# Optimization experiments

Hardware: AMD Instinct MI355X
Metric: run time of the kernel (lower is better)

Reference implementation:

```python
import jax, jax.numpy as jnp
import numpy as np

EPS = 1e-5

def layer_norm(x, g, b):
    m = jnp.mean(x, axis=-1, keepdims=True)
    v = jnp.var(x, axis=-1, keepdims=True)
    return (x - m) / jnp.sqrt(v + EPS) * g + b

def mab(Q, K, adj, Wq, Wk, Wv, Wo, g1, b1, g2, b2, H):
    # Q: [B, nq, dq], K: [B, nk, dk], adj: [nk, nk] graph-conv aggregation
    B, nq, _ = Q.shape
    dv = Wq.shape[1]
    dh = dv // H
    Qp = Q @ Wq                                   # [B, nq, dv]
    Kg = jnp.einsum('ij,bjd->bid', adj, K)        # GCN neighborhood aggregation
    Kp = Kg @ Wk                                  # [B, nk, dv]
    Vp = Kg @ Wv                                  # [B, nk, dv]
    Qh = Qp.reshape(B, nq, H, dh)
    Kh = Kp.reshape(B, -1, H, dh)
    Vh = Vp.reshape(B, -1, H, dh)
    scale = 1.0 / np.sqrt(dv).astype(np.float32)
    att = jax.nn.softmax(jnp.einsum('bqhd,bkhd->bhqk', Qh, Kh) * scale, axis=-1)
    Oh = Qh + jnp.einsum('bhqk,bkhd->bqhd', att, Vh)   # residual inside heads
    O = Oh.reshape(B, nq, dv)
    O = layer_norm(O, g1, b1)
    O = O + jax.nn.relu(O @ Wo)
    O = layer_norm(O, g2, b2)
    return O

def setup_inputs() -> dict:
    key = jax.random.key(0)
    ks = jax.random.split(key, 16)
    B, P, D = 16384, 25, 256
    w = lambda k, shp: jax.random.normal(k, shp, dtype=jnp.float32) * 0.05
    adj2 = jax.random.uniform(ks[15], (3, 3), dtype=jnp.float32)
    adj2 = adj2 / jnp.sum(adj2, axis=-1, keepdims=True)  # row-normalized GCN adj
    return {
        'X': jax.random.normal(ks[0], (B, 1, D), dtype=jnp.float32),
        'S1': w(ks[1], (3, 1)),
        'S2': w(ks[2], (P, 3)),
        'adj1': jnp.ones((1, 1), dtype=jnp.float32),
        'adj2': adj2,
        'Wq1': w(ks[3], (D, D)), 'Wk1': w(ks[4], (D, D)),
        'Wv1': w(ks[5], (D, D)), 'Wo1': w(ks[6], (D, D)),
        'g11': jnp.ones((D,), jnp.float32), 'b11': jnp.zeros((D,), jnp.float32),
        'g12': jnp.ones((D,), jnp.float32), 'b12': jnp.zeros((D,), jnp.float32),
        'Wq2': w(ks[7], (D, D)), 'Wk2': w(ks[8], (D, D)),
        'Wv2': w(ks[9], (D, D)), 'Wo2': w(ks[10], (D, D)),
        'g21': jnp.ones((D,), jnp.float32), 'b21': jnp.zeros((D,), jnp.float32),
        'g22': jnp.ones((D,), jnp.float32), 'b22': jnp.zeros((D,), jnp.float32),
        'H': 4,
    }

def reference(X, S1, S2, adj1, adj2,
              Wq1, Wk1, Wv1, Wo1, g11, b11, g12, b12,
              Wq2, Wk2, Wv2, Wo2, g21, b21, g22, b22, H):
    Q1 = jnp.einsum('ij,bjd->bid', S1, X)            # [B, 3, D]
    scale_liner = mab(Q1, X, adj1, Wq1, Wk1, Wv1, Wo1, g11, b11, g12, b12, H)
    Q2 = jnp.einsum('pj,bjd->bpd', S2, scale_liner)  # [B, 25, D]
    scale_graph = mab(Q2, scale_liner, adj2, Wq2, Wk2, Wv2, Wo2, g21, b21, g22, b22, H)
    return scale_graph
```

## Files before the change

### kernel.cpp

```cpp
#include <hip/hip_runtime.h>


typedef __attribute__((ext_vector_type(8))) short bf16x8;
typedef __attribute__((ext_vector_type(4))) float f32x4;

constexpr int D   = 256;
constexpr int AST = 264;
constexpr int SST = 264;

__device__ __forceinline__ short f2bf(float f) {
  unsigned u = __builtin_bit_cast(unsigned, f);
  u = (u + 0x7FFFu + ((u >> 16) & 1u)) >> 16;
  return (short)u;
}
__device__ __forceinline__ float bf2f(short s) {
  unsigned u = ((unsigned)(unsigned short)s) << 16;
  return __builtin_bit_cast(float, u);
}

__global__ void pack_weights(const float* __restrict__ Wq1, const float* __restrict__ Wv1,
                             const float* __restrict__ Wo1, const float* __restrict__ Wq2,
                             const float* __restrict__ Wk2, const float* __restrict__ Wv2,
                             const float* __restrict__ Wo2, short* __restrict__ ws) {
  int g = blockIdx.x * 256 + threadIdx.x;
  int mat = g >> 13, r = g & 8191;
  const float* W = (mat == 0) ? Wq1 : (mat == 1) ? Wv1 : (mat == 2) ? Wo1 :
                   (mat == 3) ? Wq2 : (mat == 4) ? Wk2 : (mat == 5) ? Wv2 : Wo2;
  int nt = r >> 9, s = (r >> 6) & 7, lane = r & 63;
  int qd = lane >> 4, mc = lane & 15;
  bf16x8 v;
#pragma unroll
  for (int j = 0; j < 8; ++j) {
    int k = s * 32 + qd * 8 + j;
    v[j] = f2bf(W[k * 256 + nt * 16 + mc]);
  }
  *reinterpret_cast<bf16x8*>(ws + (size_t)g * 8) = v;
}

template <int MT, int NTW, bool PMODE, bool SYNCMID>
__device__ __forceinline__ void wave_gemm(const short* __restrict__ ub,
                                          const bf16x8* __restrict__ Bp, int nt0,
                                          int lane, short* __restrict__ dst,
                                          int dstStride, int lim) {
  const int m = lane & 15, q = lane >> 4;
  f32x4 acc[MT][NTW];
#pragma unroll
  for (int mt = 0; mt < MT; ++mt)
#pragma unroll
    for (int n = 0; n < NTW; ++n) acc[mt][n] = (f32x4){0.f, 0.f, 0.f, 0.f};

#pragma unroll
  for (int s = 0; s < 8; ++s) {
    bf16x8 a[MT];
#pragma unroll
    for (int mt = 0; mt < MT; ++mt)
      a[mt] = *reinterpret_cast<const bf16x8*>(ub + (mt * 16 + m) * AST + s * 32 + q * 8);
#pragma unroll
    for (int n = 0; n < NTW; ++n) {
      bf16x8 b = Bp[(nt0 + n) * 512 + s * 64 + lane];
#pragma unroll
      for (int mt = 0; mt < MT; ++mt)
        acc[mt][n] = __builtin_amdgcn_mfma_f32_16x16x32_bf16(a[mt], b, acc[mt][n], 0, 0, 0);
    }
  }
  if (SYNCMID) __syncthreads();
#pragma unroll
  for (int mt = 0; mt < MT; ++mt)
#pragma unroll
    for (int n = 0; n < NTW; ++n)
#pragma unroll
      for (int r = 0; r < 4; ++r) {
        int rr = mt * 16 + q * 4 + r;
        bool ok = PMODE ? ((rr & 31) < 25) : (rr < lim);
        if (ok) dst[rr * dstStride + (nt0 + n) * 16 + m] = f2bf(acc[mt][n][r]);
      }
}

__device__ __forceinline__ void gemm_qkv(const short* __restrict__ ub,
                                         const bf16x8* __restrict__ Bp, int nt0,
                                         int lane, short* __restrict__ sb) {
  const int m = lane & 15, q = lane >> 4;
  f32x4 acc[12];
#pragma unroll
  for (int n = 0; n < 12; ++n) acc[n] = (f32x4){0.f, 0.f, 0.f, 0.f};
#pragma unroll
  for (int s = 0; s < 8; ++s) {
    bf16x8 a = *reinterpret_cast<const bf16x8*>(ub + m * AST + s * 32 + q * 8);
#pragma unroll
    for (int n = 0; n < 12; ++n) {
      bf16x8 b = Bp[(nt0 + n) * 512 + s * 64 + lane];
      acc[n] = __builtin_amdgcn_mfma_f32_16x16x32_bf16(a, b, acc[n], 0, 0, 0);
    }
  }
#pragma unroll
  for (int n = 0; n < 12; ++n) {
    int nt = nt0 + n;
    int mat = nt >> 4;
    int lo = (mat == 0) ? 0 : 6;
    int col = (nt & 15) * 16 + m;
#pragma unroll
    for (int r = 0; r < 4; ++r) {
      int rr = q * 4 + r;
      if (rr >= lo && rr < lo + 6)
        sb[(mat * 6 + rr - lo) * SST + col] = f2bf(acc[n][r]);
    }
  }
}

__device__ __forceinline__ void ln6(float (&v)[2][3], const float* __restrict__ g,
                                    const float* __restrict__ b, int tid, float* red) {
  const int lane = tid & 63, wv = tid >> 6;
#pragma unroll
  for (int i = 0; i < 6; ++i) {
    float x = v[i / 3][i % 3];
    float s = x, qq = x * x;
#pragma unroll
    for (int mm = 32; mm; mm >>= 1) {
      s += __shfl_xor(s, mm, 64);
      qq += __shfl_xor(qq, mm, 64);
    }
    if (lane == 0) {
      red[(i * 4 + wv) * 2 + 0] = s;
      red[(i * 4 + wv) * 2 + 1] = qq;
    }
  }
  __syncthreads();
  const float gg = g[tid], bb = b[tid];
#pragma unroll
  for (int i = 0; i < 6; ++i) {
    float s = red[(i * 4 + 0) * 2] + red[(i * 4 + 1) * 2] +
              red[(i * 4 + 2) * 2] + red[(i * 4 + 3) * 2];
    float qq = red[(i * 4 + 0) * 2 + 1] + red[(i * 4 + 1) * 2 + 1] +
               red[(i * 4 + 2) * 2 + 1] + red[(i * 4 + 3) * 2 + 1];
    float mean = s * (1.0f / 256.0f);
    float var  = qq * (1.0f / 256.0f) - mean * mean;
    float inv  = rsqrtf(var + 1e-5f);
    float x = v[i / 3][i % 3];
    v[i / 3][i % 3] = (x - mean) * inv * gg + bb;
  }
  __syncthreads();
}

__device__ __forceinline__ void coop_stats(const short* __restrict__ ub, int tid,
                                           float* red, float (*st)[2]) {
  const int rr = tid >> 2, part = tid & 3;
  float s = 0.f, ss = 0.f;
  if ((rr & 31) < 25) {
#pragma unroll
    for (int c = 0; c < 8; ++c) {
      bf16x8 v8 = *reinterpret_cast<const bf16x8*>(ub + rr * AST + part * 64 + c * 8);
#pragma unroll
      for (int j = 0; j < 8; ++j) {
        float f = bf2f(v8[j]);
        s += f;
        ss = fmaf(f, f, ss);
      }
    }
  }
  red[(rr * 4 + part) * 2 + 0] = s;
  red[(rr * 4 + part) * 2 + 1] = ss;
  __syncthreads();
  if (tid < 64) {
    float S = 0.f, SS = 0.f;
#pragma unroll
    for (int i = 0; i < 4; ++i) {
      S  += red[(tid * 4 + i) * 2 + 0];
      SS += red[(tid * 4 + i) * 2 + 1];
    }
    float mean = S * (1.0f / 256.0f);
    float var  = SS * (1.0f / 256.0f) - mean * mean;
    st[tid][0] = mean;
    st[tid][1] = rsqrtf(var + 1e-5f);
  }
}

__global__ __launch_bounds__(256, 3)
void gt_mfma(const float* __restrict__ X, const float* __restrict__ S1,
             const float* __restrict__ S2, const float* __restrict__ adj1,
             const float* __restrict__ adj2,
             const float* __restrict__ g11, const float* __restrict__ b11,
             const float* __restrict__ g12, const float* __restrict__ b12,
             const float* __restrict__ g21, const float* __restrict__ b21,
             const float* __restrict__ g22, const float* __restrict__ b22,
             const short* __restrict__ wsp, float* __restrict__ out) {
  __shared__ __align__(16) short ubuf[64 * AST];
  __shared__ __align__(16) short sbuf[18 * SST];
  __shared__ __align__(16) float wbuf[4][64][4];
  __shared__ float slkbuf[4][6][3];
  __shared__ float stbuf[64][2];
  __shared__ float redbuf[512];

  const int tid = threadIdx.x, lane = tid & 63, wv = tid >> 6;
  const int b0 = blockIdx.x * 2;

  const bf16x8* pQV1 = (const bf16x8*)(wsp + 0 * 65536);
  const bf16x8* pWo1 = (const bf16x8*)(wsp + 2 * 65536);
  const bf16x8* pQKV = (const bf16x8*)(wsp + 3 * 65536);
  const bf16x8* pWo2 = (const bf16x8*)(wsp + 6 * 65536);

  short* qv = sbuf + 6 * SST;

  float x0 = X[(size_t)(b0 + 0) * D + tid];
  float x1 = X[(size_t)(b0 + 1) * D + tid];
  ubuf[0 * AST + tid] = f2bf(x0);
  ubuf[1 * AST + tid] = f2bf(x1);
  __syncthreads();

  wave_gemm<1, 8, false, false>(ubuf, pQV1, wv * 8, lane, qv, 528, 2);
  __syncthreads();

  const float a1 = adj1[0];
  float o1[2][3];
#pragma unroll
  for (int b = 0; b < 2; ++b) {
    float xq = bf2f(qv[b * 528 + tid]);
    float xv = bf2f(qv[b * 528 + 256 + tid]) * a1;
#pragma unroll
    for (int qq = 0; qq < 3; ++qq) o1[b][qq] = fmaf(S1[qq], xq, xv);
  }
  ln6(o1, g11, b11, tid, redbuf);

#pragma unroll
  for (int b = 0; b < 2; ++b)
#pragma unroll
    for (int qq = 0; qq < 3; ++qq) ubuf[(b * 3 + qq) * AST + tid] = f2bf(o1[b][qq]);
  __syncthreads();
  wave_gemm<1, 4, false, false>(ubuf, pWo1, wv * 4, lane, sbuf, SST, 6);
  __syncthreads();
#pragma unroll
  for (int b = 0; b < 2; ++b)
#pragma unroll
    for (int qq = 0; qq < 3; ++qq)
      o1[b][qq] += fmaxf(bf2f(sbuf[(b * 3 + qq) * SST + tid]), 0.f);
  ln6(o1, g12, b12, tid, redbuf);

#pragma unroll
  for (int b = 0; b < 2; ++b)
#pragma unroll
    for (int qq = 0; qq < 3; ++qq) ubuf[(b * 3 + qq) * AST + tid] = f2bf(o1[b][qq]);
#pragma unroll
  for (int b = 0; b < 2; ++b)
#pragma unroll
    for (int i = 0; i < 3; ++i) {
      float kg = adj2[i * 3 + 0] * o1[b][0] + adj2[i * 3 + 1] * o1[b][1] +
                 adj2[i * 3 + 2] * o1[b][2];
      ubuf[(6 + b * 3 + i) * AST + tid] = f2bf(kg);
    }
  __syncthreads();

  gemm_qkv(ubuf, pQKV, wv * 12, lane, sbuf);
  __syncthreads();

  {
    const int m = lane & 15, q = lane >> 4;
    f32x4 sa = (f32x4){0.f, 0.f, 0.f, 0.f};
#pragma unroll
    for (int s = 0; s < 2; ++s) {
      bf16x8 aq = *reinterpret_cast<const bf16x8*>(
          sbuf + m * SST + wv * 64 + s * 32 + q * 8);
      bf16x8 bk = (bf16x8){0, 0, 0, 0, 0, 0, 0, 0};
      if (m < 6)
        bk = *reinterpret_cast<const bf16x8*>(
            sbuf + (6 + m) * SST + wv * 64 + s * 32 + q * 8);
      sa = __builtin_amdgcn_mfma_f32_16x16x32_bf16(aq, bk, sa, 0, 0, 0);
    }
#pragma unroll
    for (int r = 0; r < 4; ++r) {
      int i = q * 4 + r;
      if (i < 6 && m < 6 && ((i >= 3) == (m >= 3)))
        slkbuf[wv][i][m % 3] = sa[r] * 0.0625f;
    }
    int b = lane >> 5, p = lane & 31;
    if (p < 25) {
      float sc0 = 0.f, sc1 = 0.f, sc2 = 0.f;
#pragma unroll
      for (int ii = 0; ii < 3; ++ii) {
        float s2v = S2[p * 3 + ii];
        sc0 = fmaf(s2v, slkbuf[wv][b * 3 + ii][0], sc0);
        sc1 = fmaf(s2v, slkbuf[wv][b * 3 + ii][1], sc1);
        sc2 = fmaf(s2v, slkbuf[wv][b * 3 + ii][2], sc2);
      }
      float mx = fmaxf(sc0, fmaxf(sc1, sc2));
      float e0 = __expf(sc0 - mx), e1 = __expf(sc1 - mx), e2 = __expf(sc2 - mx);
      float inv = 1.f / (e0 + e1 + e2);
      wbuf[wv][b * 32 + p][0] = e0 * inv;
      wbuf[wv][b * 32 + p][1] = e1 * inv;
      wbuf[wv][b * 32 + p][2] = e2 * inv;
      wbuf[wv][b * 32 + p][3] = 0.f;
    }
  }
  __syncthreads();

  float accv[2][25];
#pragma unroll
  for (int b = 0; b < 2; ++b) {
    float slq0 = bf2f(sbuf[(b * 3 + 0) * SST + tid]);
    float slq1 = bf2f(sbuf[(b * 3 + 1) * SST + tid]);
    float slq2 = bf2f(sbuf[(b * 3 + 2) * SST + tid]);
    float vp0 = bf2f(sbuf[(12 + b * 3 + 0) * SST + tid]);
    float vp1 = bf2f(sbuf[(12 + b * 3 + 1) * SST + tid]);
    float vp2 = bf2f(sbuf[(12 + b * 3 + 2) * SST + tid]);
#pragma unroll
    for (int p = 0; p < 25; ++p) {
      float4 w4 = *reinterpret_cast<const float4*>(&wbuf[wv][b * 32 + p][0]);
      float qpv = S2[p * 3 + 0] * slq0 + S2[p * 3 + 1] * slq1 + S2[p * 3 + 2] * slq2;
      float x = qpv + w4.x * vp0 + w4.y * vp1 + w4.z * vp2;
      accv[b][p] = x;
      ubuf[(b * 32 + p) * AST + tid] = f2bf(x);
    }
  }
  __syncthreads();

  coop_stats(ubuf, tid, redbuf, stbuf);
  __syncthreads();
  {
    const float gg = g21[tid], bb2 = b21[tid];
#pragma unroll
    for (int b = 0; b < 2; ++b)
#pragma unroll
      for (int p = 0; p < 25; ++p) {
        int rr = b * 32 + p;
        accv[b][p] = (accv[b][p] - stbuf[rr][0]) * stbuf[rr][1] * gg + bb2;
      }
  }

#pragma unroll
  for (int b = 0; b < 2; ++b)
#pragma unroll
    for (int p = 0; p < 25; ++p) ubuf[(b * 32 + p) * AST + tid] = f2bf(accv[b][p]);
  __syncthreads();
  wave_gemm<2, 4, true, true>(ubuf, pWo2, wv * 4, lane, ubuf, AST, 0);
  wave_gemm<2, 4, true, true>(ubuf + 32 * AST, pWo2, wv * 4, lane, ubuf + 32 * AST, AST, 0);
  __syncthreads();

#pragma unroll
  for (int b = 0; b < 2; ++b)
#pragma unroll
    for (int p = 0; p < 25; ++p) {
      float r = bf2f(ubuf[(b * 32 + p) * AST + tid]);
      float x = accv[b][p] + fmaxf(r, 0.f);
      accv[b][p] = x;
      ubuf[(b * 32 + p) * AST + tid] = f2bf(x);
    }
  __syncthreads();
  coop_stats(ubuf, tid, redbuf, stbuf);
  __syncthreads();
  {
    const float gg = g22[tid], bb2 = b22[tid];
#pragma unroll
    for (int b = 0; b < 2; ++b)
#pragma unroll
      for (int p = 0; p < 25; ++p) {
        int rr = b * 32 + p;
        float v = (accv[b][p] - stbuf[rr][0]) * stbuf[rr][1] * gg + bb2;
        out[((size_t)(b0 + b) * 25 + p) * D + tid] = v;
      }
  }
}

extern "C" void kernel_launch(void* const* d_in, const int* in_sizes, int n_in,
                              void* d_out, int out_size, void* d_ws, size_t ws_size,
                              hipStream_t stream) {
  const float* X    = (const float*)d_in[0];
  const float* S1   = (const float*)d_in[1];
  const float* S2   = (const float*)d_in[2];
  const float* adj1 = (const float*)d_in[3];
  const float* adj2 = (const float*)d_in[4];
  const float* Wq1  = (const float*)d_in[5];
  const float* Wv1  = (const float*)d_in[7];
  const float* Wo1  = (const float*)d_in[8];
  const float* g11  = (const float*)d_in[9];
  const float* b11  = (const float*)d_in[10];
  const float* g12  = (const float*)d_in[11];
  const float* b12  = (const float*)d_in[12];
  const float* Wq2  = (const float*)d_in[13];
  const float* Wk2  = (const float*)d_in[14];
  const float* Wv2  = (const float*)d_in[15];
  const float* Wo2  = (const float*)d_in[16];
  const float* g21  = (const float*)d_in[17];
  const float* b21  = (const float*)d_in[18];
  const float* g22  = (const float*)d_in[19];
  const float* b22  = (const float*)d_in[20];

  short* wsp = (short*)d_ws;

  hipLaunchKernelGGL(pack_weights, dim3(224), dim3(256), 0, stream,
                     Wq1, Wv1, Wo1, Wq2, Wk2, Wv2, Wo2, wsp);

  const int B = in_sizes[0] / D;
  hipLaunchKernelGGL(gt_mfma, dim3(B / 2), dim3(256), 0, stream,
                     X, S1, S2, adj1, adj2, g11, b11, g12, b12,
                     g21, b21, g22, b22, (const short*)wsp, (float*)d_out);
}
```

Before: 972.6 us.

## Process stage-two batches sequentially to halve LDS and registers, raise occupancy

The second MAB stage now loops over the two batch elements one at a time, using a 32-row activation buffer and a 25-entry accumulator instead of 64 rows and 50 entries. The row-statistics reduction is replaced by an 8-lane shuffle reduction, which drops one shared-memory round trip and one barrier. Launch bounds go from 3 to 5 blocks per multiprocessor to exploit the lower LDS and register footprint. The cost is more barriers and less independent work per block in that phase, and the earlier stages still use the smaller ubuf, which must fit.

```diff
diff --git a/kernel.cpp b/kernel.cpp
--- a/kernel.cpp
+++ b/kernel.cpp
@@ -141,14 +141,14 @@
   __syncthreads();
 }
 
-__device__ __forceinline__ void coop_stats(const short* __restrict__ ub, int tid,
-                                           float* red, float (*st)[2]) {
-  const int rr = tid >> 2, part = tid & 3;
+__device__ __forceinline__ void coop_stats32(const short* __restrict__ ub, int tid,
+                                             float (*st)[2]) {
+  const int rr = tid >> 3, part = tid & 7;
   float s = 0.f, ss = 0.f;
-  if ((rr & 31) < 25) {
-#pragma unroll
-    for (int c = 0; c < 8; ++c) {
-      bf16x8 v8 = *reinterpret_cast<const bf16x8*>(ub + rr * AST + part * 64 + c * 8);
+  if (rr < 25) {
+#pragma unroll
+    for (int c = 0; c < 4; ++c) {
+      bf16x8 v8 = *reinterpret_cast<const bf16x8*>(ub + rr * AST + part * 32 + c * 8);
 #pragma unroll
       for (int j = 0; j < 8; ++j) {
         float f = bf2f(v8[j]);
@@ -157,24 +157,20 @@
       }
     }
   }
-  red[(rr * 4 + part) * 2 + 0] = s;
-  red[(rr * 4 + part) * 2 + 1] = ss;
-  __syncthreads();
-  if (tid < 64) {
-    float S = 0.f, SS = 0.f;
-#pragma unroll
-    for (int i = 0; i < 4; ++i) {
-      S  += red[(tid * 4 + i) * 2 + 0];
-      SS += red[(tid * 4 + i) * 2 + 1];
-    }
-    float mean = S * (1.0f / 256.0f);
-    float var  = SS * (1.0f / 256.0f) - mean * mean;
-    st[tid][0] = mean;
-    st[tid][1] = rsqrtf(var + 1e-5f);
-  }
-}
-
-__global__ __launch_bounds__(256, 3)
+#pragma unroll
+  for (int mm = 4; mm; mm >>= 1) {
+    s  += __shfl_xor(s, mm, 64);
+    ss += __shfl_xor(ss, mm, 64);
+  }
+  if (part == 0 && rr < 25) {
+    float mean = s * (1.0f / 256.0f);
+    float var  = ss * (1.0f / 256.0f) - mean * mean;
+    st[rr][0] = mean;
+    st[rr][1] = rsqrtf(var + 1e-5f);
+  }
+}
+
+__global__ __launch_bounds__(256, 5)
 void gt_mfma(const float* __restrict__ X, const float* __restrict__ S1,
              const float* __restrict__ S2, const float* __restrict__ adj1,
              const float* __restrict__ adj2,
@@ -183,12 +179,12 @@
              const float* __restrict__ g21, const float* __restrict__ b21,
              const float* __restrict__ g22, const float* __restrict__ b22,
              const short* __restrict__ wsp, float* __restrict__ out) {
-  __shared__ __align__(16) short ubuf[64 * AST];
+  __shared__ __align__(16) short ubuf[32 * AST];
   __shared__ __align__(16) short sbuf[18 * SST];
   __shared__ __align__(16) float wbuf[4][64][4];
   __shared__ float slkbuf[4][6][3];
-  __shared__ float stbuf[64][2];
-  __shared__ float redbuf[512];
+  __shared__ float stbuf[32][2];
+  __shared__ float redbuf[64];
 
   const int tid = threadIdx.x, lane = tid & 63, wv = tid >> 6;
   const int b0 = blockIdx.x * 2;
@@ -291,70 +287,62 @@
   }
   __syncthreads();
 
-  float accv[2][25];
-#pragma unroll
   for (int b = 0; b < 2; ++b) {
-    float slq0 = bf2f(sbuf[(b * 3 + 0) * SST + tid]);
-    float slq1 = bf2f(sbuf[(b * 3 + 1) * SST + tid]);
-    float slq2 = bf2f(sbuf[(b * 3 + 2) * SST + tid]);
-    float vp0 = bf2f(sbuf[(12 + b * 3 + 0) * SST + tid]);
-    float vp1 = bf2f(sbuf[(12 + b * 3 + 1) * SST + tid]);
-    float vp2 = bf2f(sbuf[(12 + b * 3 + 2) * SST + tid]);
+    float accv[25];
+    {
+      float slq0 = bf2f(sbuf[(b * 3 + 0) * SST + tid]);
+      float slq1 = bf2f(sbuf[(b * 3 + 1) * SST + tid]);
+      float slq2 = bf2f(sbuf[(b * 3 + 2) * SST + tid]);
+      float vp0 = bf2f(sbuf[(12 + b * 3 + 0) * SST + tid]);
+      float vp1 = bf2f(sbuf[(12 + b * 3 + 1) * SST + tid]);
+      float vp2 = bf2f(sbuf[(12 + b * 3 + 2) * SST + tid]);
+#pragma unroll
+      for (int p = 0; p < 25; ++p) {
+        float4 w4 = *reinterpret_cast<const float4*>(&wbuf[wv][b * 32 + p][0]);
+        float qpv = S2[p * 3 + 0] * slq0 + S2[p * 3 + 1] * slq1 + S2[p * 3 + 2] * slq2;
+        float x = qpv + w4.x * vp0 + w4.y * vp1 + w4.z * vp2;
+        accv[p] = x;
+        ubuf[p * AST + tid] = f2bf(x);
+      }
+    }
+    __syncthreads();
+
+    coop_stats32(ubuf, tid, stbuf);
+    __syncthreads();
+    {
+      const float gg = g21[tid], bb2 = b21[tid];
+#pragma unroll
+      for (int p = 0; p < 25; ++p) {
+        float x = (accv[p] - stbuf[p][0]) * stbuf[p][1] * gg + bb2;
+        accv[p] = x;
+        ubuf[p * AST + tid] = f2bf(x);
+      }
+    }
+    __syncthreads();
+
+    wave_gemm<2, 4, true, true>(ubuf, pWo2, wv * 4, lane, ubuf, AST, 0);
+    __syncthreads();
+
 #pragma unroll
     for (int p = 0; p < 25; ++p) {
-      float4 w4 = *reinterpret_cast<const float4*>(&wbuf[wv][b * 32 + p][0]);
-      float qpv = S2[p * 3 + 0] * slq0 + S2[p * 3 + 1] * slq1 + S2[p * 3 + 2] * slq2;
-      float x = qpv + w4.x * vp0 + w4.y * vp1 + w4.z * vp2;
-      accv[b][p] = x;
-      ubuf[(b * 32 + p) * AST + tid] = f2bf(x);
-    }
-  }
-  __syncthreads();
-
-  coop_stats(ubuf, tid, redbuf, stbuf);
-  __syncthreads();
-  {
-    const float gg = g21[tid], bb2 = b21[tid];
-#pragma unroll
-    for (int b = 0; b < 2; ++b)
+      float r = bf2f(ubuf[p * AST + tid]);
+      float x = accv[p] + fmaxf(r, 0.f);
+      accv[p] = x;
+      ubuf[p * AST + tid] = f2bf(x);
+    }
+    __syncthreads();
+
+    coop_stats32(ubuf, tid, stbuf);
+    __syncthreads();
+    {
+      const float gg = g22[tid], bb2 = b22[tid];
 #pragma unroll
       for (int p = 0; p < 25; ++p) {
-        int rr = b * 32 + p;
-        accv[b][p] = (accv[b][p] - stbuf[rr][0]) * stbuf[rr][1] * gg + bb2;
-      }
-  }
-
-#pragma unroll
-  for (int b = 0; b < 2; ++b)
-#pragma unroll
-    for (int p = 0; p < 25; ++p) ubuf[(b * 32 + p) * AST + tid] = f2bf(accv[b][p]);
-  __syncthreads();
-  wave_gemm<2, 4, true, true>(ubuf, pWo2, wv * 4, lane, ubuf, AST, 0);
-  wave_gemm<2, 4, true, true>(ubuf + 32 * AST, pWo2, wv * 4, lane, ubuf + 32 * AST, AST, 0);
-  __syncthreads();
-
-#pragma unroll
-  for (int b = 0; b < 2; ++b)
-#pragma unroll
-    for (int p = 0; p < 25; ++p) {
-      float r = bf2f(ubuf[(b * 32 + p) * AST + tid]);
-      float x = accv[b][p] + fmaxf(r, 0.f);
-      accv[b][p] = x;
-      ubuf[(b * 32 + p) * AST + tid] = f2bf(x);
-    }
-  __syncthreads();
-  coop_stats(ubuf, tid, redbuf, stbuf);
-  __syncthreads();
-  {
-    const float gg = g22[tid], bb2 = b22[tid];
-#pragma unroll
-    for (int b = 0; b < 2; ++b)
-#pragma unroll
-      for (int p = 0; p < 25; ++p) {
-        int rr = b * 32 + p;
-        float v = (accv[b][p] - stbuf[rr][0]) * stbuf[rr][1] * gg + bb2;
+        float v = (accv[p] - stbuf[p][0]) * stbuf[p][1] * gg + bb2;
         out[((size_t)(b0 + b) * 25 + p) * D + tid] = v;
       }
+    }
+    __syncthreads();
   }
 }
 
```

New measurement: 1.353 ms. 1.39x slower.
